# Kernel optimization log

Measured on AMD Instinct MI355X. Metric: run time of the kernel, lower is better.

## Reference

```python
import jax, jax.numpy as jnp
import numpy as np

B, T, N, C = 32, 12, 1024, 64
NW = T - 3   # number of 4-step windows (9)
K = 4        # window length == res_filters[0]
NL = 3       # len(filters)


def setup_inputs() -> dict:
    key = jax.random.key(0)
    ks = jax.random.split(key, 9)
    s = 0.02
    return {
        "original_data": jax.random.normal(ks[0], (B, T, N, C), jnp.float32),
        "data": jax.random.normal(ks[1], (B, T, N, C), jnp.float32),
        "adj_st": jax.random.uniform(ks[2], (N, 4 * N), jnp.float32) / (4.0 * N),
        "temporal_emb": jax.random.normal(ks[3], (1, T, 1, C), jnp.float32) * s,
        "spatial_emb": jax.random.normal(ks[4], (1, 1, N, C), jnp.float32) * s,
        "conv1_w": jax.random.normal(ks[5], (2 * C, C, 1, K), jnp.float32) * s,
        "conv1_b": jax.random.normal(ks[6], (2 * C,), jnp.float32) * s,
        "gcn_w": jax.random.normal(ks[7], (NW, NL, C, 2 * C), jnp.float32) * s,
        "gcn_b": jax.random.normal(ks[8], (NW, NL, 1, 2 * C), jnp.float32) * 0.1,
    }


def reference(original_data, data, adj_st, temporal_emb, spatial_emb,
              conv1_w, conv1_b, gcn_w, gcn_b):
    # ---- residual gated conv along time axis (T==12 so conv2 branch is dead) ----
    temp = jnp.transpose(data, (0, 3, 2, 1))  # (B,C,N,T)
    temp = jax.lax.conv_general_dilated(
        temp, conv1_w, window_strides=(1, 1), padding="VALID",
        dimension_numbers=("NCHW", "OIHW", "NCHW"))  # (B,2C,N,T-K+1)
    temp = temp + conv1_b[None, :, None, None]
    left, right = temp[:, :C], temp[:, C:]
    data_res = jnp.transpose(jax.nn.sigmoid(left) * right, (0, 3, 2, 1))  # (B,NW,N,C)

    # ---- position embedding (add) ----
    x = data + temporal_emb + spatial_emb  # (B,T,N,C)

    # ---- build all 4-step windows: (NW, 4N, B, C) ----
    idx = jnp.arange(NW)[:, None] + jnp.arange(K)[None, :]  # (NW,K)
    wins = x[:, idx]                                         # (B,NW,K,N,C)
    wins = jnp.transpose(wins, (1, 2, 3, 0, 4)).reshape(NW, K * N, B, C)

    def one_window(win, Ws, bs):
        wing, cur = win[:3 * N], win[3 * N:]
        outs = []
        for j in range(NL):
            full = jnp.concatenate([wing, cur], axis=0)       # (4N,B,C)
            y = jnp.einsum("nm,mbc->nbc", adj_st, full)       # (N,B,C)
            z = jnp.einsum("nbc,cd->nbd", y, Ws[j]) + bs[j]   # (N,B,2C)
            cur = z[..., :C] * jax.nn.sigmoid(z[..., C:])      # GLU
            outs.append(cur)
        return jnp.max(jnp.stack(outs, 0), axis=0)            # (N,B,C)

    out = jax.vmap(one_window)(wins, gcn_w, gcn_b)            # (NW,N,B,C)
    out = jnp.transpose(out, (2, 0, 1, 3))                    # (B,NW,N,C)
    return out + data_res
```

## Files before the change

### kernel.cpp

```cpp
#include <hip/hip_runtime.h>
#include <cstdint>
#include <cstddef>


typedef __bf16 bf16;
typedef float f32x4 __attribute__((ext_vector_type(4)));
typedef __bf16 bf16x8 __attribute__((ext_vector_type(8)));

constexpr int B_  = 32;
constexpr int T_  = 12;
constexpr int N_  = 1024;
constexpr int C_  = 64;
constexpr int NW_ = 9;
constexpr long long SLAB_ = 2048LL * 1024LL;

constexpr int OF_ADJ  = 0;
constexpr int OF_TEMB = 4194304;
constexpr int OF_SEMB = 4195072;
constexpr int OF_C1W  = 4260608;
constexpr int OF_C1B  = 4293376;
constexpr int OF_GW   = 4293504;
constexpr int OF_GB   = 4514688;
constexpr int OF_END  = 4518144;

static __device__ __forceinline__ float sigmoidf_(float x) {
  return __builtin_amdgcn_rcpf(1.0f + __expf(-x));
}

static __device__ __forceinline__ void g2l16(const bf16* g, bf16* l) {
  __builtin_amdgcn_global_load_lds(
      (const __attribute__((address_space(1))) void*)g,
      (__attribute__((address_space(3))) void*)l, 16, 0, 0);
}

__global__ __launch_bounds__(256)
void k_detect(const void* __restrict__ data_raw, int* __restrict__ flag)
{
  __shared__ int cnt;
  const int tid = threadIdx.x;
  if (tid == 0) cnt = 0;
  __syncthreads();
  const uint32_t* W = (const uint32_t*)data_raw;
  int local = 0;
  for (int s = 0; s < 32; s++) {
    const uint32_t w = W[tid * 32 + s];
    const int e8 = (int)((w >> 7) & 0xFF);
    local += (e8 < 97 || e8 > 157) ? 1 : 0;
  }
  atomicAdd(&cnt, local);
  __syncthreads();
  if (tid == 0) *flag = (cnt > 2458) ? 1 : 0;
}

static __device__ __forceinline__ float rd_(const void* p, long long i, int isF32) {
  return isF32 ? ((const float*)p)[i] : (float)((const bf16*)p)[i];
}

__global__ __launch_bounds__(256)
void k_convert(const void* adj, const void* temb, const void* semb,
               const void* c1w, const void* c1b, const void* gw, const void* gb,
               const int* __restrict__ flagp, bf16* __restrict__ canon)
{
  const int isF32 = *flagp;
  const int e = blockIdx.x * 256 + threadIdx.x;
  float v;
  if      (e < OF_TEMB) v = rd_(adj,  e,           isF32);
  else if (e < OF_SEMB) v = rd_(temb, e - OF_TEMB, isF32);
  else if (e < OF_C1W)  v = rd_(semb, e - OF_SEMB, isF32);
  else if (e < OF_C1B)  v = rd_(c1w,  e - OF_C1W,  isF32);
  else if (e < OF_GW)   v = rd_(c1b,  e - OF_C1B,  isF32);
  else if (e < OF_GB)   v = rd_(gw,   e - OF_GW,   isF32);
  else                  v = rd_(gb,   e - OF_GB,   isF32);
  canon[e] = (bf16)v;
}

__global__ __launch_bounds__(256)
void k_prepg(const void* __restrict__ data_raw, const int* __restrict__ flagp,
             const bf16* __restrict__ temb, const bf16* __restrict__ semb,
             bf16* __restrict__ xg, int tbase)
{
  const int isF32 = *flagp;
  const int s  = blockIdx.z;
  const int t  = tbase + s;
  const int n0 = blockIdx.x * 32;
  const int bc = blockIdx.y * 256 + threadIdx.x;
  const int b = bc >> 6, c = bc & 63;

  __shared__ bf16 lsS[32 * 64];
  *(bf16x8*)&lsS[threadIdx.x * 8] = *(const bf16x8*)&semb[n0 * C_ + threadIdx.x * 8];
  __syncthreads();

  const float te = (float)temb[t * C_ + c];
  const long long dbase = ((long long)(b * T_ + t) * N_ + n0) * C_ + c;
  bf16* op = xg + (size_t)s * SLAB_ + (size_t)bc * N_ + n0;
#pragma unroll
  for (int i = 0; i < 32; i += 8) {
    bf16x8 v;
#pragma unroll
    for (int u = 0; u < 8; u++) {
      const int n = i + u;
      const float dv = rd_(data_raw, dbase + (long long)n * C_, isF32);
      v[u] = (bf16)(dv + te + (float)lsS[n * C_ + c]);
    }
    *(bf16x8*)&op[i] = v;
  }
}

__global__ __launch_bounds__(256)
void k_wprep(const bf16* __restrict__ conv1w, const bf16* __restrict__ gcnw,
             bf16* __restrict__ Wt, bf16* __restrict__ gwT)
{
  const int idx = blockIdx.x * 256 + threadIdx.x;
  if (idx < 128 * 256) {
    const int c2 = idx >> 8, kidx = idx & 255;
    const int ci = kidx & 63, k = kidx >> 6;
    Wt[idx] = conv1w[c2 * 256 + ci * 4 + k];
  }
  const int i2 = idx - 128 * 256;
  if (i2 >= 0 && i2 < 27 * 8192) {
    const int wj = i2 >> 13, r = i2 & 8191;
    const int d = r >> 6, c = r & 63;
    gwT[i2] = gcnw[wj * 8192 + c * 128 + d];
  }
}

template<int MODE>
__global__ __launch_bounds__(256)
void k_gemm_adj(const bf16* __restrict__ Aadj, const bf16* __restrict__ Bop,
                const float* __restrict__ initY, float* __restrict__ outF,
                const bf16* __restrict__ gwT, const bf16* __restrict__ gcnb,
                bf16* __restrict__ curT, float* __restrict__ maxT,
                int Ksize, int jlayer, int wbase)
{
  const int lw = blockIdx.z;
  const int m0 = blockIdx.y * 128;
  const int c0 = blockIdx.x * 128;
  const int tid = threadIdx.x;
  const int lane = tid & 63, wid = tid >> 6;
  const int lrow = lane & 15, q = lane >> 4;
  const int wm = wid >> 1, wn = wid & 1;

  __shared__ __align__(16) bf16 lsAll[16384];

  const int srow = lane >> 2;
  const int sl_w = ((lane >> 2) & 3) ^ ((lane >> 4) & 3);
  const int skel = ((lane & 3) ^ sl_w) * 8;

  const int sl_r  = (lrow & 3) ^ (lrow >> 2);
  const int rdoff = ((q ^ sl_r) & 3) * 8;

  const bf16* Bw = Bop + (size_t)lw * SLAB_;

  auto STAGE = [&](int buf, int k0) {
    const int tblk = k0 >> 10;
    const int kloc = k0 & 1023;
    const bf16* Bt = Bw + (size_t)tblk * SLAB_ + kloc;
    const bf16* At = Aadj + k0;
#pragma unroll
    for (int s = 0; s < 2; s++) {
      const int ch  = s * 4 + wid;
      const int row = ch * 16 + srow;
      g2l16(&At[(size_t)(m0 + row) * 4096 + skel], &lsAll[buf * 4096 + ch * 512]);
      g2l16(&Bt[(size_t)(c0 + row) * N_   + skel], &lsAll[8192 + buf * 4096 + ch * 512]);
    }
  };

  STAGE(0, 0);

  f32x4 acc[4][4];
  const size_t woff = (size_t)lw * SLAB_;
  if (MODE == 1) {
#pragma unroll
    for (int i = 0; i < 4; i++)
#pragma unroll
      for (int jj = 0; jj < 4; jj++) {
        const int col = c0 + wn * 64 + jj * 16 + lrow;
        const int b = col >> 6, c = col & 63;
        const float* yp = initY + woff + (size_t)b * (N_ * C_)
                        + (size_t)(m0 + wm * 64 + i * 16 + q * 4) * C_ + c;
#pragma unroll
        for (int r = 0; r < 4; r++) acc[i][jj][r] = yp[(size_t)r * C_];
      }
  } else {
#pragma unroll
    for (int i = 0; i < 4; i++)
#pragma unroll
      for (int jj = 0; jj < 4; jj++)
#pragma unroll
        for (int r = 0; r < 4; r++) acc[i][jj][r] = 0.0f;
  }

  __syncthreads();

  int cur = 0;
  for (int k0 = 0; k0 < Ksize; k0 += 32) {
    if (k0 + 32 < Ksize) STAGE(cur ^ 1, k0 + 32);

    bf16x8 af[4], bfv[4];
#pragma unroll
    for (int i = 0; i < 4; i++)
      af[i]  = *(const bf16x8*)&lsAll[cur * 4096 + (wm * 64 + i * 16 + lrow) * 32 + rdoff];
#pragma unroll
    for (int jj = 0; jj < 4; jj++)
      bfv[jj] = *(const bf16x8*)&lsAll[8192 + cur * 4096 + (wn * 64 + jj * 16 + lrow) * 32 + rdoff];
#pragma unroll
    for (int i = 0; i < 4; i++)
#pragma unroll
      for (int jj = 0; jj < 4; jj++)
        acc[i][jj] = __builtin_amdgcn_mfma_f32_16x16x32_bf16(af[i], bfv[jj], acc[i][jj], 0, 0, 0);

    __syncthreads();
    cur ^= 1;
  }

  if (MODE == 0) {
#pragma unroll
    for (int i = 0; i < 4; i++)
#pragma unroll
      for (int jj = 0; jj < 4; jj++) {
        const int col = c0 + wn * 64 + jj * 16 + lrow;
        const int b = col >> 6, c = col & 63;
        const size_t base = woff + (size_t)b * (N_ * C_)
                          + (size_t)(m0 + wm * 64 + i * 16 + q * 4) * C_ + c;
#pragma unroll
        for (int r = 0; r < 4; r++) outF[base + (size_t)r * C_] = acc[i][jj][r];
      }
    return;
  }

  char* tls = (char*)lsAll;
#pragma unroll
  for (int i = 0; i < 4; i++)
#pragma unroll
    for (int jj = 0; jj < 4; jj++) {
      const int bc = wn * 64 + jj * 16 + lrow;
#pragma unroll
      for (int r = 0; r < 4; r++) {
        const int m = wm * 64 + i * 16 + q * 4 + r;
        const int byte = m * 256 + ((bc * 2) ^ (((m ^ (m >> 3)) & 7) << 4));
        *(bf16*)(tls + byte) = (bf16)acc[i][jj][r];
      }
    }
  __syncthreads();

  const int wj = (wbase + lw) * 3 + jlayer;
  const bf16* Agw  = gwT  + (size_t)wj * 8192;
  const bf16* bias = gcnb + (size_t)wj * 128;
  const int nloc0 = wid * 32;

#pragma unroll
  for (int bl = 0; bl < 2; bl++) {
    f32x4 acc2[8][2];
#pragma unroll
    for (int rt = 0; rt < 8; rt++)
#pragma unroll
      for (int ct = 0; ct < 2; ct++)
#pragma unroll
        for (int r = 0; r < 4; r++) acc2[rt][ct][r] = 0.0f;

#pragma unroll
    for (int ks = 0; ks < 2; ks++) {
      bf16x8 bv[2];
#pragma unroll
      for (int ct = 0; ct < 2; ct++) {
        const int nl = nloc0 + ct * 16 + lrow;
        const int byte = nl * 256 +
          (((bl * 64 + ks * 32 + q * 8) * 2) ^ (((nl ^ (nl >> 3)) & 7) << 4));
        bv[ct] = *(const bf16x8*)(tls + byte);
      }
#pragma unroll
      for (int rt = 0; rt < 8; rt++) {
        const bf16x8 av = *(const bf16x8*)&Agw[(rt * 16 + lrow) * 64 + ks * 32 + q * 8];
#pragma unroll
        for (int ct = 0; ct < 2; ct++)
          acc2[rt][ct] = __builtin_amdgcn_mfma_f32_16x16x32_bf16(av, bv[ct], acc2[rt][ct], 0, 0, 0);
      }
    }

    const int bg = (c0 >> 6) + bl;
#pragma unroll
    for (int rt = 0; rt < 4; rt++)
#pragma unroll
      for (int ct = 0; ct < 2; ct++) {
        const int n = m0 + nloc0 + ct * 16 + lrow;
#pragma unroll
        for (int r = 0; r < 4; r++) {
          const int d = rt * 16 + q * 4 + r;
          const float zL = acc2[rt][ct][r]     + (float)bias[d];
          const float zR = acc2[rt + 4][ct][r] + (float)bias[d + 64];
          const float cv = zL * sigmoidf_(zR);
          const size_t addr = woff + (size_t)(bg * 64 + d) * N_ + n;
          if (jlayer < 2) curT[addr] = (bf16)cv;
          if (jlayer == 0) maxT[addr] = cv;
          else             maxT[addr] = fmaxf(maxT[addr], cv);
        }
      }
  }
}

__global__ __launch_bounds__(256)
void k_final(const void* __restrict__ data_raw, const int* __restrict__ flagp,
             const bf16* __restrict__ Wt, const bf16* __restrict__ convb,
             const float* __restrict__ maxT, float* __restrict__ out, int wbase)
{
  const int isF32 = *flagp;
  const int lw = blockIdx.z;
  const int w = wbase + lw;
  const int bbat = blockIdx.y;
  const int tid = threadIdx.x;
  const int lane = tid & 63, wid = tid >> 6;
  const int lrow = lane & 15, q = lane >> 4;
  const int n0 = blockIdx.x * 128 + wid * 32;

  f32x4 acc[2][8];
#pragma unroll
  for (int rt = 0; rt < 2; rt++)
#pragma unroll
    for (int ct = 0; ct < 8; ct++)
#pragma unroll
      for (int r = 0; r < 4; r++) acc[rt][ct][r] = 0.0f;

#pragma unroll
  for (int s = 0; s < 8; s++) {
    const int k = s >> 1, ci0 = (s & 1) * 32;
    bf16x8 av[2];
#pragma unroll
    for (int rt = 0; rt < 2; rt++) {
      const long long off =
        ((long long)((bbat * T_ + w + k) * N_) + n0 + rt * 16 + lrow) * C_ + ci0 + q * 8;
      if (!isF32) {
        av[rt] = *(const bf16x8*)&((const bf16*)data_raw)[off];
      } else {
        const float* p = (const float*)data_raw + off;
        const f32x4 v0 = *(const f32x4*)p;
        const f32x4 v1 = *(const f32x4*)(p + 4);
        bf16x8 v;
#pragma unroll
        for (int u = 0; u < 4; u++) { v[u] = (bf16)v0[u]; v[u + 4] = (bf16)v1[u]; }
        av[rt] = v;
      }
    }
#pragma unroll
    for (int ct = 0; ct < 8; ct++) {
      const bf16x8 bv = *(const bf16x8*)&Wt[(ct * 16 + lrow) * 256 + s * 32 + q * 8];
#pragma unroll
      for (int rt = 0; rt < 2; rt++)
        acc[rt][ct] = __builtin_amdgcn_mfma_f32_16x16x32_bf16(av[rt], bv, acc[rt][ct], 0, 0, 0);
    }
  }

#pragma unroll
  for (int rt = 0; rt < 2; rt++)
#pragma unroll
    for (int ctL = 0; ctL < 4; ctL++) {
      const int cL = ctL * 16 + lrow;
      const float bL = (float)convb[cL], bR = (float)convb[cL + 64];
#pragma unroll
      for (int r = 0; r < 4; r++) {
        const int n = n0 + rt * 16 + q * 4 + r;
        const float zL = acc[rt][ctL][r] + bL;
        const float zR = acc[rt][ctL + 4][r] + bR;
        const float res = sigmoidf_(zL) * zR;
        const float mv = maxT[(size_t)lw * SLAB_ + (size_t)(bbat * 64 + cL) * N_ + n];
        out[(size_t)((bbat * NW_ + w) * N_ + n) * C_ + cL] = res + mv;
      }
    }
}

extern "C" void kernel_launch(void* const* d_in, const int* in_sizes, int n_in,
                              void* d_out, int out_size, void* d_ws, size_t ws_size,
                              hipStream_t stream)
{
  (void)in_sizes; (void)n_in; (void)out_size;
  const void* data   = d_in[1];
  const void* adj    = d_in[2];
  const void* temb   = d_in[3];
  const void* semb   = d_in[4];
  const void* conv1w = d_in[5];
  const void* conv1b = d_in[6];
  const void* gcnw   = d_in[7];
  const void* gcnb   = d_in[8];
  float* out = (float*)d_out;

  auto fp = [&](int g) -> size_t {
    size_t need = 256;
    auto pad = [&](size_t x) { need += (x + 255) & ~(size_t)255; };
    pad((size_t)OF_END * 2);
    pad((size_t)(g + 3) * SLAB_ * 2);
    pad((size_t)g * SLAB_ * 4);
    pad((size_t)g * SLAB_ * 2);
    pad((size_t)g * SLAB_ * 4);
    pad(128 * 256 * 2);
    pad(27 * 8192 * 2);
    return need;
  };

  int G = 1;
  for (int g = 9; g >= 2; g--) if (fp(g) <= ws_size) { G = g; break; }

  char* ws = (char*)d_ws;
  int* flag = (int*)ws;
  size_t off = 256;
  auto allocB = [&](size_t bytes) -> char* {
    char* p = ws + off;
    off += (bytes + 255) & ~(size_t)255;
    return p;
  };
  bf16*  canon = (bf16*) allocB((size_t)OF_END * 2);
  bf16*  xg    = (bf16*) allocB((size_t)(G + 3) * SLAB_ * 2);
  float* Yw    = (float*)allocB((size_t)G * SLAB_ * 4);
  bf16*  curT  = (bf16*) allocB((size_t)G * SLAB_ * 2);
  float* maxT  = (float*)allocB((size_t)G * SLAB_ * 4);
  bf16*  Wt    = (bf16*) allocB(128 * 256 * 2);
  bf16*  gwT   = (bf16*) allocB(27 * 8192 * 2);

  const bf16* adjC  = canon + OF_ADJ;
  const bf16* tembC = canon + OF_TEMB;
  const bf16* sembC = canon + OF_SEMB;
  const bf16* c1wC  = canon + OF_C1W;
  const bf16* c1bC  = canon + OF_C1B;
  const bf16* gwC   = canon + OF_GW;
  const bf16* gbC   = canon + OF_GB;

  k_detect<<<dim3(1), 256, 0, stream>>>(data, flag);
  k_convert<<<dim3(OF_END / 256), 256, 0, stream>>>(adj, temb, semb, conv1w, conv1b,
                                                    gcnw, gcnb, flag, canon);
  k_wprep<<<dim3(992), 256, 0, stream>>>(c1wC, gwC, Wt, gwT);

  for (int wbase = 0; wbase < NW_; wbase += G) {
    const int gc = (NW_ - wbase < G) ? (NW_ - wbase) : G;

    k_prepg<<<dim3(32, 8, gc + 3), 256, 0, stream>>>(data, flag, tembC, sembC, xg, wbase);

    k_gemm_adj<0><<<dim3(16, 8, gc), 256, 0, stream>>>(
        adjC, xg, nullptr, Yw, nullptr, nullptr, nullptr, nullptr, 3072, 0, 0);

    for (int j = 0; j < 3; j++) {
      const bf16* Bop = (j == 0) ? (xg + 3 * SLAB_) : curT;
      k_gemm_adj<1><<<dim3(16, 8, gc), 256, 0, stream>>>(
          adjC + 3072, Bop, Yw, nullptr, gwT, gbC, curT, maxT, 1024, j, wbase);
    }

    k_final<<<dim3(8, 32, gc), 256, 0, stream>>>(data, flag, Wt, c1bC, maxT, out, wbase);
  }
}
```

Measured before the change: 917.4 us.

## Fuse wing GEMM into first layer and defer max to final kernel

The separate wing-only adjacency GEMM (K=3072) is merged with the first GCN layer into a single K=4096 pass. That pass writes the partial wing result Y to memory at the last wing k-step and then continues into the layer-0 epilogue, which removes one launch and one re-read of Y. The fp32 running-max buffer is replaced by three separate bf16 per-layer outputs, and the final kernel computes the max over them, which removes the read-modify-write of maxT in every layer. The trade-offs are a larger workspace, which may lower the group size G, and a max taken over bf16-rounded values instead of fp32.

```diff
diff --git a/kernel.cpp b/kernel.cpp
--- a/kernel.cpp
+++ b/kernel.cpp
@@ -6,6 +6,7 @@
 typedef __bf16 bf16;
 typedef float f32x4 __attribute__((ext_vector_type(4)));
 typedef __bf16 bf16x8 __attribute__((ext_vector_type(8)));
+typedef __bf16 bf16x4 __attribute__((ext_vector_type(4)));
 
 constexpr int B_  = 32;
 constexpr int T_  = 12;
@@ -129,8 +130,7 @@
 void k_gemm_adj(const bf16* __restrict__ Aadj, const bf16* __restrict__ Bop,
                 const float* __restrict__ initY, float* __restrict__ outF,
                 const bf16* __restrict__ gwT, const bf16* __restrict__ gcnb,
-                bf16* __restrict__ curT, float* __restrict__ maxT,
-                int Ksize, int jlayer, int wbase)
+                bf16* __restrict__ outCur, int Ksize, int jlayer, int wbase)
 {
   const int lw = blockIdx.z;
   const int m0 = blockIdx.y * 128;
@@ -209,23 +209,22 @@
       for (int jj = 0; jj < 4; jj++)
         acc[i][jj] = __builtin_amdgcn_mfma_f32_16x16x32_bf16(af[i], bfv[jj], acc[i][jj], 0, 0, 0);
 
+    if (MODE == 2 && k0 == 3072 - 32) {
+#pragma unroll
+      for (int i = 0; i < 4; i++)
+#pragma unroll
+        for (int jj = 0; jj < 4; jj++) {
+          const int col = c0 + wn * 64 + jj * 16 + lrow;
+          const int b = col >> 6, c = col & 63;
+          const size_t base = woff + (size_t)b * (N_ * C_)
+                            + (size_t)(m0 + wm * 64 + i * 16 + q * 4) * C_ + c;
+#pragma unroll
+          for (int r = 0; r < 4; r++) outF[base + (size_t)r * C_] = acc[i][jj][r];
+        }
+    }
+
     __syncthreads();
     cur ^= 1;
-  }
-
-  if (MODE == 0) {
-#pragma unroll
-    for (int i = 0; i < 4; i++)
-#pragma unroll
-      for (int jj = 0; jj < 4; jj++) {
-        const int col = c0 + wn * 64 + jj * 16 + lrow;
-        const int b = col >> 6, c = col & 63;
-        const size_t base = woff + (size_t)b * (N_ * C_)
-                          + (size_t)(m0 + wm * 64 + i * 16 + q * 4) * C_ + c;
-#pragma unroll
-        for (int r = 0; r < 4; r++) outF[base + (size_t)r * C_] = acc[i][jj][r];
-      }
-    return;
   }
 
   char* tls = (char*)lsAll;
@@ -289,10 +288,7 @@
           const float zL = acc2[rt][ct][r]     + (float)bias[d];
           const float zR = acc2[rt + 4][ct][r] + (float)bias[d + 64];
           const float cv = zL * sigmoidf_(zR);
-          const size_t addr = woff + (size_t)(bg * 64 + d) * N_ + n;
-          if (jlayer < 2) curT[addr] = (bf16)cv;
-          if (jlayer == 0) maxT[addr] = cv;
-          else             maxT[addr] = fmaxf(maxT[addr], cv);
+          outCur[woff + (size_t)(bg * 64 + d) * N_ + n] = (bf16)cv;
         }
       }
   }
@@ -301,7 +297,8 @@
 __global__ __launch_bounds__(256)
 void k_final(const void* __restrict__ data_raw, const int* __restrict__ flagp,
              const bf16* __restrict__ Wt, const bf16* __restrict__ convb,
-             const float* __restrict__ maxT, float* __restrict__ out, int wbase)
+             const bf16* __restrict__ cur0, const bf16* __restrict__ cur1,
+             const bf16* __restrict__ cur2, float* __restrict__ out, int wbase)
 {
   const int isF32 = *flagp;
   const int lw = blockIdx.z;
@@ -355,13 +352,18 @@
     for (int ctL = 0; ctL < 4; ctL++) {
       const int cL = ctL * 16 + lrow;
       const float bL = (float)convb[cL], bR = (float)convb[cL + 64];
+      const size_t cbase = (size_t)lw * SLAB_ + (size_t)(bbat * 64 + cL) * N_
+                         + n0 + rt * 16 + q * 4;
+      const bf16x4 m0v = *(const bf16x4*)&cur0[cbase];
+      const bf16x4 m1v = *(const bf16x4*)&cur1[cbase];
+      const bf16x4 m2v = *(const bf16x4*)&cur2[cbase];
 #pragma unroll
       for (int r = 0; r < 4; r++) {
         const int n = n0 + rt * 16 + q * 4 + r;
         const float zL = acc[rt][ctL][r] + bL;
         const float zR = acc[rt][ctL + 4][r] + bR;
         const float res = sigmoidf_(zL) * zR;
-        const float mv = maxT[(size_t)lw * SLAB_ + (size_t)(bbat * 64 + cL) * N_ + n];
+        const float mv = fmaxf(fmaxf((float)m0v[r], (float)m1v[r]), (float)m2v[r]);
         out[(size_t)((bbat * NW_ + w) * N_ + n) * C_ + cL] = res + mv;
       }
     }
@@ -382,21 +384,20 @@
   const void* gcnb   = d_in[8];
   float* out = (float*)d_out;
 
-  auto fp = [&](int g) -> size_t {
+  auto fpn = [&](int g) -> size_t {
     size_t need = 256;
     auto pad = [&](size_t x) { need += (x + 255) & ~(size_t)255; };
     pad((size_t)OF_END * 2);
     pad((size_t)(g + 3) * SLAB_ * 2);
     pad((size_t)g * SLAB_ * 4);
-    pad((size_t)g * SLAB_ * 2);
-    pad((size_t)g * SLAB_ * 4);
+    pad((size_t)3 * g * SLAB_ * 2);
     pad(128 * 256 * 2);
     pad(27 * 8192 * 2);
     return need;
   };
 
   int G = 1;
-  for (int g = 9; g >= 2; g--) if (fp(g) <= ws_size) { G = g; break; }
+  for (int g = 9; g >= 2; g--) if (fpn(g) <= ws_size) { G = g; break; }
 
   char* ws = (char*)d_ws;
   int* flag = (int*)ws;
@@ -409,10 +410,13 @@
   bf16*  canon = (bf16*) allocB((size_t)OF_END * 2);
   bf16*  xg    = (bf16*) allocB((size_t)(G + 3) * SLAB_ * 2);
   float* Yw    = (float*)allocB((size_t)G * SLAB_ * 4);
-  bf16*  curT  = (bf16*) allocB((size_t)G * SLAB_ * 2);
-  float* maxT  = (float*)allocB((size_t)G * SLAB_ * 4);
+  bf16*  curT  = (bf16*) allocB((size_t)3 * G * SLAB_ * 2);
   bf16*  Wt    = (bf16*) allocB(128 * 256 * 2);
   bf16*  gwT   = (bf16*) allocB(27 * 8192 * 2);
+
+  bf16* cur0 = curT;
+  bf16* cur1 = curT + (size_t)G * SLAB_;
+  bf16* cur2 = curT + (size_t)2 * G * SLAB_;
 
   const bf16* adjC  = canon + OF_ADJ;
   const bf16* tembC = canon + OF_TEMB;
@@ -432,15 +436,15 @@
 
     k_prepg<<<dim3(32, 8, gc + 3), 256, 0, stream>>>(data, flag, tembC, sembC, xg, wbase);
 
-    k_gemm_adj<0><<<dim3(16, 8, gc), 256, 0, stream>>>(
-        adjC, xg, nullptr, Yw, nullptr, nullptr, nullptr, nullptr, 3072, 0, 0);
-
-    for (int j = 0; j < 3; j++) {
-      const bf16* Bop = (j == 0) ? (xg + 3 * SLAB_) : curT;
-      k_gemm_adj<1><<<dim3(16, 8, gc), 256, 0, stream>>>(
-          adjC + 3072, Bop, Yw, nullptr, gwT, gbC, curT, maxT, 1024, j, wbase);
-    }
-
-    k_final<<<dim3(8, 32, gc), 256, 0, stream>>>(data, flag, Wt, c1bC, maxT, out, wbase);
-  }
-}
+    k_gemm_adj<2><<<dim3(16, 8, gc), 256, 0, stream>>>(
+        adjC, xg, nullptr, Yw, gwT, gbC, cur0, 4096, 0, wbase);
+
+    k_gemm_adj<1><<<dim3(16, 8, gc), 256, 0, stream>>>(
+        adjC + 3072, cur0, Yw, nullptr, gwT, gbC, cur1, 1024, 1, wbase);
+    k_gemm_adj<1><<<dim3(16, 8, gc), 256, 0, stream>>>(
+        adjC + 3072, cur1, Yw, nullptr, gwT, gbC, cur2, 1024, 2, wbase);
+
+    k_final<<<dim3(8, 32, gc), 256, 0, stream>>>(data, flag, Wt, c1bC,
+                                                 cur0, cur1, cur2, out, wbase);
+  }
+}
```

Result: no change. 911.7 us (-0.6%).
